# Optimization experiments

Measured on AMD Instinct MI355X. Metric: run time of the kernel, lower is better.

## Reference

```python
import jax, jax.numpy as jnp
import numpy as np

B, T, D = 2, 2048, 2048
H, KV = 16, 4
HD = D // H            # 128
N_REP = H // KV        # 4
KV_DIM = D * KV // H   # 512
ALIBI_W = 0.1


def _rotate_half(x):
    x1, x2 = jnp.split(x, 2, axis=-1)
    return jnp.concatenate([-x2, x1], axis=-1)


def _apply_rope(xq, xk, freqs_cis):
    # xq: [B,H,T,hd], xk: [B,KV,T,hd]; freqs_cis: [T, hd] (cos half | sin half)
    seq_len, head_dim = xq.shape[2], xq.shape[3]
    freqs = freqs_cis[:seq_len, :]
    half = head_dim // 2
    cos = jnp.repeat(freqs[:, :half], 2, axis=-1)[None, None]  # [1,1,T,hd]
    sin = jnp.repeat(freqs[:, half:], 2, axis=-1)[None, None]
    xq_out = xq * cos + _rotate_half(xq) * sin
    xk_out = xk * cos + _rotate_half(xk) * sin
    return xq_out, xk_out


def setup_inputs() -> dict:
    key = jax.random.key(0)
    ks = jax.random.split(key, 8)
    x = jax.random.normal(ks[0], (B, T, D), jnp.float32)
    # additive causal mask (0 on/below diag, -1e9 above)
    causal = jnp.tril(jnp.ones((T, T), jnp.bool_))
    mask = jnp.where(causal, 0.0, -1e9).astype(jnp.float32)[None, None]
    # RoPE table: first half cos, second half sin of t*theta
    inv_freq = 1.0 / (10000.0 ** (np.arange(0, HD, 2, dtype=np.float32) / HD))  # [hd/2]
    angles = jnp.arange(T, dtype=jnp.float32)[:, None] * jnp.asarray(inv_freq)[None, :]
    freqs_cis = jnp.concatenate([jnp.cos(angles), jnp.sin(angles)], axis=-1)  # [T, hd]
    # ALiBi bias: per-head slope * relative distance
    slopes = 2.0 ** (-8.0 * (jnp.arange(1, H + 1, dtype=jnp.float32) / H))  # [H]
    rel = (jnp.arange(T, dtype=jnp.float32)[None, :] - jnp.arange(T, dtype=jnp.float32)[:, None])
    alibi_bias = (-jnp.abs(rel)[None, None] * slopes[None, :, None, None]).astype(jnp.float32)
    std = 0.02
    Wq = std * jax.random.normal(ks[1], (D, D), jnp.float32)
    Wk = std * jax.random.normal(ks[2], (D, KV_DIM), jnp.float32)
    Wv = std * jax.random.normal(ks[3], (D, KV_DIM), jnp.float32)
    Wo = std * jax.random.normal(ks[4], (D, D), jnp.float32)
    return {"x": x, "mask": mask, "freqs_cis": freqs_cis, "alibi_bias": alibi_bias,
            "Wq": Wq, "Wk": Wk, "Wv": Wv, "Wo": Wo}


def reference(x, mask, freqs_cis, alibi_bias, Wq, Wk, Wv, Wo):
    b, t, d = x.shape
    q = (x @ Wq).reshape(b, t, H, HD).transpose(0, 2, 1, 3)      # [B,H,T,hd]
    k = (x @ Wk).reshape(b, t, KV, HD).transpose(0, 2, 1, 3)     # [B,KV,T,hd]
    v = (x @ Wv).reshape(b, t, KV, HD).transpose(0, 2, 1, 3)     # [B,KV,T,hd]
    q, k = _apply_rope(q, k, freqs_cis)
    # grouped-query scores: group query heads by kv head, avoid repeating K/V
    qg = q.reshape(b, KV, N_REP, t, HD)
    scores = jnp.einsum('bgrtd,bgsd->bgrts', qg, k) / jnp.sqrt(jnp.float32(HD))
    alibi = alibi_bias[:, :, :t, :t].reshape(1, KV, N_REP, t, t)
    scores = scores * (1.0 - ALIBI_W) + alibi * ALIBI_W
    scores = scores + mask[:, :, None, :t, :t]                   # broadcast [1,1,1,T,T]
    attn = jax.nn.softmax(scores.astype(jnp.float32), axis=-1).astype(x.dtype)
    out = jnp.einsum('bgrts,bgsd->bgrtd', attn, v)               # [B,KV,n_rep,T,hd]
    out = out.reshape(b, H, t, HD).transpose(0, 2, 1, 3).reshape(b, t, d)
    return out @ Wo
```

## Files before the change

### kernel.cpp

```cpp
#include <hip/hip_runtime.h>

#define T_SEQ 2048
#define D_MODEL 2048
#define NH 16
#define NKV 4
#define HEAD_DIM 128

typedef unsigned short u16;
typedef __attribute__((ext_vector_type(8))) short bf16x8;
typedef __attribute__((ext_vector_type(4))) float f32x4;

__device__ __forceinline__ float bf2f(u16 u) { return __uint_as_float(((unsigned)u) << 16); }
__device__ __forceinline__ u16 f2bf(float f) {
  unsigned x = __float_as_uint(f);
  return (u16)((x + 0x7FFFu + ((x >> 16) & 1u)) >> 16);
}
__device__ __forceinline__ float fexp2(float x) { return __builtin_amdgcn_exp2f(x); }

#define ASYNC_COPY16(g, l)                                                        \
  __builtin_amdgcn_global_load_lds((const __attribute__((address_space(1))) unsigned int*)(g), \
                                   (__attribute__((address_space(3))) unsigned int*)(l), 16, 0, 0)

#define BARRIER() do { asm volatile("" ::: "memory"); __builtin_amdgcn_s_barrier(); asm volatile("" ::: "memory"); } while (0)

__global__ void cast_kernel(const float* __restrict__ x, u16* __restrict__ y, int n4) {
  int i = blockIdx.x * 256 + threadIdx.x;
  if (i >= n4) return;
  const float4 v = reinterpret_cast<const float4*>(x)[i];
  unsigned p0 = (unsigned)f2bf(v.x) | ((unsigned)f2bf(v.y) << 16);
  unsigned p1 = (unsigned)f2bf(v.z) | ((unsigned)f2bf(v.w) << 16);
  reinterpret_cast<uint2*>(y)[i] = make_uint2(p0, p1);
}

__global__ void transpose_kernel(const float* __restrict__ W, u16* __restrict__ WT, int K, int N) {
  __shared__ float t[32][33];
  int n0 = blockIdx.x * 32, k0 = blockIdx.y * 32;
  int tx = threadIdx.x, ty = threadIdx.y;
#pragma unroll
  for (int i = 0; i < 32; i += 8)
    t[ty + i][tx] = W[(size_t)(k0 + ty + i) * N + n0 + tx];
  __syncthreads();
#pragma unroll
  for (int i = 0; i < 32; i += 8)
    WT[(size_t)(n0 + ty + i) * K + k0 + tx] = f2bf(t[tx][ty + i]);
}

__global__ void vt_kernel(const u16* __restrict__ vb, u16* __restrict__ vt, int vstride) {
  __shared__ u16 t[32][33];
  const int bg = blockIdx.z;
  const int b = bg >> 2, g = bg & 3;
  const int t0 = blockIdx.x * 32, n0 = blockIdx.y * 32;
  const int tx = threadIdx.x, ty = threadIdx.y;
#pragma unroll
  for (int i = 0; i < 32; i += 8)
    t[ty + i][tx] = vb[((size_t)(b * T_SEQ + t0 + ty + i)) * vstride + g * HEAD_DIM + n0 + tx];
  __syncthreads();
#pragma unroll
  for (int i = 0; i < 32; i += 8)
    vt[((size_t)(bg * HEAD_DIM + n0 + ty + i)) * T_SEQ + t0 + tx] = t[tx][ty + i];
}

template<int OUT_BF16>
__global__ __launch_bounds__(512, 1) void gemm256(const u16* __restrict__ A, const u16* __restrict__ BT,
                                                  void* __restrict__ Cv, int M, int N, int K) {
  __shared__ u16 S[4][256 * 64];
  const int tid = threadIdx.x;
  const int wave = tid >> 6, lane = tid & 63;
  const int lr = lane & 15, lg = lane >> 4;
  const int wm = wave >> 2, wn = wave & 3;
  const size_t arow0 = (size_t)blockIdx.y * 256;
  const size_t brow0 = (size_t)blockIdx.x * 256;
  const int NT = K >> 6;

  const int srow_in_w = lane >> 3;
  const int scol = ((lane & 7) ^ srow_in_w) << 3;

  f32x4 acc[8][4] = {};
  bf16x8 af[4][2], bf0[2][2], bf1[2][2];

  auto stage = [&](int mat, int half, int ktile, int buf) {
    if (ktile >= NT) return;
    const u16* gb = mat ? (BT + brow0 * K) : (A + arow0 * K);
    const int kcol = ktile << 6;
#pragma unroll
    for (int i = 0; i < 2; ++i) {
      const int row = half * 128 + i * 64 + wave * 8 + srow_in_w;
      const u16* src = gb + (size_t)row * K + kcol + scol;
      u16* dst = &S[buf * 2 + mat][(half * 128 + i * 64 + wave * 8) * 64];
      ASYNC_COPY16(src, dst);
    }
  };
  auto ldA = [&](int c, int mh) {
#pragma unroll
    for (int m4 = 0; m4 < 4; ++m4)
#pragma unroll
      for (int ks = 0; ks < 2; ++ks)
        af[m4][ks] = *reinterpret_cast<const bf16x8*>(
            &S[c * 2][(wm * 128 + (mh * 4 + m4) * 16 + lr) * 64 + ((((ks << 2) | lg) ^ (lane & 7)) << 3)]);
  };
  auto ldB = [&](int c, int nh, bf16x8 (*bfr)[2]) {
#pragma unroll
    for (int n2 = 0; n2 < 2; ++n2)
#pragma unroll
      for (int ks = 0; ks < 2; ++ks)
        bfr[n2][ks] = *reinterpret_cast<const bf16x8*>(
            &S[c * 2 + 1][(wn * 64 + (nh * 2 + n2) * 16 + lr) * 64 + ((((ks << 2) | lg) ^ (lane & 7)) << 3)]);
  };
  auto mfmaQ = [&](int mh, int nh, bf16x8 (*bfr)[2]) {
    __builtin_amdgcn_s_setprio(1);
#pragma unroll
    for (int m4 = 0; m4 < 4; ++m4)
#pragma unroll
      for (int n2 = 0; n2 < 2; ++n2)
#pragma unroll
        for (int ks = 0; ks < 2; ++ks)
          acc[mh * 4 + m4][nh * 2 + n2] = __builtin_amdgcn_mfma_f32_16x16x32_bf16(
              af[m4][ks], bfr[n2][ks], acc[mh * 4 + m4][nh * 2 + n2], 0, 0, 0);
    __builtin_amdgcn_s_setprio(0);
  };

  stage(0, 0, 0, 0); stage(0, 1, 0, 0); stage(1, 0, 0, 0); stage(1, 1, 0, 0);
  stage(1, 0, 1, 1); stage(0, 0, 1, 1);
  asm volatile("s_waitcnt vmcnt(4)" ::: "memory");
  BARRIER();

  for (int kt = 0; kt < NT; ++kt) {
    const int c = kt & 1;
    ldA(c, 0); ldB(c, 0, bf0);
    stage(0, 1, kt + 1, c ^ 1);
    BARRIER();
    mfmaQ(0, 0, bf0);
    BARRIER();
    ldB(c, 1, bf1);
    stage(1, 1, kt + 1, c ^ 1);
    BARRIER();
    mfmaQ(0, 1, bf1);
    BARRIER();
    ldA(c, 1);
    stage(1, 0, kt + 2, c);
    BARRIER();
    mfmaQ(1, 1, bf1);
    BARRIER();
    stage(0, 0, kt + 2, c);
    BARRIER();
    mfmaQ(1, 0, bf0);
    if (kt + 2 < NT) { asm volatile("s_waitcnt vmcnt(4)" ::: "memory"); }
    else             { asm volatile("s_waitcnt vmcnt(0)" ::: "memory"); }
    BARRIER();
  }

#pragma unroll
  for (int mf = 0; mf < 8; ++mf)
#pragma unroll
    for (int nf = 0; nf < 4; ++nf)
#pragma unroll
      for (int r = 0; r < 4; ++r) {
        size_t row = arow0 + wm * 128 + mf * 16 + lg * 4 + r;
        size_t col = brow0 + wn * 64 + nf * 16 + lr;
        if (OUT_BF16) ((u16*)Cv)[row * N + col] = f2bf(acc[mf][nf][r]);
        else          ((float*)Cv)[row * N + col] = acc[mf][nf][r];
      }
}

__global__ void rope_kernel(u16* __restrict__ q, const float* __restrict__ freqs, int log2nh,
                            int stride, int total) {
  int idx = blockIdx.x * 256 + threadIdx.x;
  if (idx >= total) return;
  int d = idx & 63;
  int h = (idx >> 6) & ((1 << log2nh) - 1);
  int row = idx >> (6 + log2nh);
  int t = row & (T_SEQ - 1);
  size_t base = (size_t)row * stride + (size_t)h * 128;
  float x1 = bf2f(q[base + d]);
  float x2 = bf2f(q[base + 64 + d]);
  const float* fr = freqs + (size_t)t * 128;
  int dh = d >> 1;
  float c1 = fr[dh],      s1 = fr[64 + dh];
  float c2 = fr[32 + dh], s2 = fr[96 + dh];
  q[base + d]      = f2bf(x1 * c1 - x2 * s1);
  q[base + 64 + d] = f2bf(x2 * c2 + x1 * s2);
}

__global__ __launch_bounds__(512) void attn_kernel(const u16* __restrict__ q, const u16* __restrict__ k,
                                                   const u16* __restrict__ vt, u16* __restrict__ o,
                                                   int qstride, int kstride) {
  __shared__ u16 Kl[2][64][136];
  __shared__ u16 Vl[2][128][72];
  __shared__ u16 Pl[8][16][72];
  const int b = blockIdx.z, h = blockIdx.y, pairIdx = blockIdx.x;
  const int g = h >> 2;
  const int tid = threadIdx.x, wave = tid >> 6, lane = tid & 63;
  const int lr = lane & 15, lg = lane >> 4;

  const float LOG2E = 1.44269504089f;
  const float qk_scale = 0.9f / sqrtf(128.f) * LOG2E;
  const float slope2   = 0.1f * fexp2(-0.5f * (h + 1)) * LOG2E;
  const float THR = 16.0f;

  const int krow = tid >> 3, kc0 = (tid & 7) * 16;
  const int vrow = tid >> 2, vc0 = (tid & 3) * 16;
  const u16* kbp = k + ((size_t)(b * T_SEQ + krow)) * kstride + g * HEAD_DIM + kc0;
  const u16* vbp = vt + ((size_t)((b * NKV + g) * HEAD_DIM + vrow)) * T_SEQ + vc0;

  float cb[4];
#pragma unroll
  for (int nt = 0; nt < 4; ++nt) cb[nt] = slope2 * (float)(nt * 16 + lr);

  for (int half = 0; half < 2; ++half) {
    const int qt = half ? (15 - pairIdx) : pairIdx;
    const int qbase = qt * 128;

    const u16* qp = q + ((size_t)(b * T_SEQ + qbase + wave * 16 + lr)) * qstride + h * HEAD_DIM;
    bf16x8 qf[4];
#pragma unroll
    for (int ks = 0; ks < 4; ++ks) qf[ks] = *reinterpret_cast<const bf16x8*>(qp + ks * 32 + lg * 8);

    f32x4 oa[8] = {};
    float m_r[4], l_r[4];
#pragma unroll
    for (int r = 0; r < 4; ++r) { m_r[r] = -1e30f; l_r[r] = 0.f; }

    const int ktmax = 2 * qt + 1;
    const int irow_min_w = qbase + wave * 16;
    const int irow_max_w = irow_min_w + 15;
    int cur = 0;

    __syncthreads();
    {
      bf16x8 k0a = *reinterpret_cast<const bf16x8*>(kbp);
      bf16x8 k0b = *reinterpret_cast<const bf16x8*>(kbp + 8);
      bf16x8 v0a = *reinterpret_cast<const bf16x8*>(vbp);
      bf16x8 v0b = *reinterpret_cast<const bf16x8*>(vbp + 8);
      *reinterpret_cast<bf16x8*>(&Kl[0][krow][kc0]) = k0a;
      *reinterpret_cast<bf16x8*>(&Kl[0][krow][kc0 + 8]) = k0b;
      *reinterpret_cast<bf16x8*>(&Vl[0][vrow][vc0]) = v0a;
      *reinterpret_cast<bf16x8*>(&Vl[0][vrow][vc0 + 8]) = v0b;
    }

    for (int kt = 0; kt <= ktmax; ++kt) {
      const int kbase = kt * 64;
      __syncthreads();

      const bool pf = (kt < ktmax);
      bf16x8 pk0, pk1, pv0, pv1;
      if (pf) {
        const u16* ks2p = kbp + (size_t)(kbase + 64) * kstride;
        pk0 = *reinterpret_cast<const bf16x8*>(ks2p);
        pk1 = *reinterpret_cast<const bf16x8*>(ks2p + 8);
        const u16* vs2p = vbp + kbase + 64;
        pv0 = *reinterpret_cast<const bf16x8*>(vs2p);
        pv1 = *reinterpret_cast<const bf16x8*>(vs2p + 8);
      }

      const bool compute = (kbase <= irow_max_w);
      if (compute) {
        f32x4 sa[4] = {};
#pragma unroll
        for (int nt = 0; nt < 4; ++nt)
#pragma unroll
          for (int ks = 0; ks < 4; ++ks)
            sa[nt] = __builtin_amdgcn_mfma_f32_16x16x32_bf16(
                qf[ks], *reinterpret_cast<const bf16x8*>(&Kl[cur][nt * 16 + lr][ks * 32 + lg * 8]), sa[nt], 0, 0, 0);

        const int i_row0 = irow_min_w + lg * 4;
        const float tb = slope2 * (float)kbase;
        float sv[4][4];
        float pmx[4] = {-1e30f, -1e30f, -1e30f, -1e30f};
        if (kbase + 63 <= irow_min_w) {
#pragma unroll
          for (int nt = 0; nt < 4; ++nt) {
            const float bias = cb[nt] + tb;
#pragma unroll
            for (int r = 0; r < 4; ++r) {
              float xv = fmaf(sa[nt][r], qk_scale, bias);
              sv[nt][r] = xv;
              pmx[r] = fmaxf(pmx[r], xv);
            }
          }
        } else {
#pragma unroll
          for (int nt = 0; nt < 4; ++nt) {
            const int jcol = kbase + nt * 16 + lr;
            const float bias = cb[nt] + tb;
#pragma unroll
            for (int r = 0; r < 4; ++r) {
              float xv = (jcol <= i_row0 + r) ? fmaf(sa[nt][r], qk_scale, bias) : -1e30f;
              sv[nt][r] = xv;
              pmx[r] = fmaxf(pmx[r], xv);
            }
          }
        }

        bool okl = true;
#pragma unroll
        for (int r = 0; r < 4; ++r) okl = okl && (pmx[r] <= m_r[r] + THR);
        if (__all(okl)) {
          float rs[4] = {0.f, 0.f, 0.f, 0.f};
#pragma unroll
          for (int nt = 0; nt < 4; ++nt)
#pragma unroll
            for (int r = 0; r < 4; ++r) {
              float p = fexp2(sv[nt][r] - m_r[r]);
              sv[nt][r] = p;
              rs[r] += p;
            }
#pragma unroll
          for (int r = 0; r < 4; ++r) l_r[r] += rs[r];
        } else {
#pragma unroll
          for (int mm = 1; mm < 16; mm <<= 1)
#pragma unroll
            for (int r = 0; r < 4; ++r) pmx[r] = fmaxf(pmx[r], __shfl_xor(pmx[r], mm, 64));
          float corr[4], rs[4];
#pragma unroll
          for (int r = 0; r < 4; ++r) {
            float mn = fmaxf(m_r[r], pmx[r]);
            corr[r] = fexp2(m_r[r] - mn);
            m_r[r] = mn;
            rs[r] = 0.f;
          }
#pragma unroll
          for (int nt = 0; nt < 4; ++nt)
#pragma unroll
            for (int r = 0; r < 4; ++r) {
              float p = fexp2(sv[nt][r] - m_r[r]);
              sv[nt][r] = p;
              rs[r] += p;
            }
#pragma unroll
          for (int r = 0; r < 4; ++r) l_r[r] = l_r[r] * corr[r] + rs[r];
#pragma unroll
          for (int t8 = 0; t8 < 8; ++t8)
#pragma unroll
            for (int r = 0; r < 4; ++r) oa[t8][r] *= corr[r];
        }

#pragma unroll
        for (int nt = 0; nt < 4; ++nt)
#pragma unroll
          for (int r = 0; r < 4; ++r)
            Pl[wave][lg * 4 + r][nt * 16 + lr] = f2bf(sv[nt][r]);
      }

      if (pf) {
        *reinterpret_cast<bf16x8*>(&Kl[cur ^ 1][krow][kc0]) = pk0;
        *reinterpret_cast<bf16x8*>(&Kl[cur ^ 1][krow][kc0 + 8]) = pk1;
        *reinterpret_cast<bf16x8*>(&Vl[cur ^ 1][vrow][vc0]) = pv0;
        *reinterpret_cast<bf16x8*>(&Vl[cur ^ 1][vrow][vc0 + 8]) = pv1;
      }

      if (compute) {
#pragma unroll
        for (int ht = 0; ht < 8; ++ht)
#pragma unroll
          for (int ks2 = 0; ks2 < 2; ++ks2) {
            bf16x8 pa = *reinterpret_cast<const bf16x8*>(&Pl[wave][lr][ks2 * 32 + lg * 8]);
            bf16x8 vb8 = *reinterpret_cast<const bf16x8*>(&Vl[cur][ht * 16 + lr][ks2 * 32 + lg * 8]);
            oa[ht] = __builtin_amdgcn_mfma_f32_16x16x32_bf16(pa, vb8, oa[ht], 0, 0, 0);
          }
      }
      cur ^= 1;
    }

#pragma unroll
    for (int mm = 1; mm < 16; mm <<= 1)
#pragma unroll
      for (int r = 0; r < 4; ++r) l_r[r] += __shfl_xor(l_r[r], mm, 64);

    u16* op = o + ((size_t)(b * T_SEQ + qbase + wave * 16)) * D_MODEL + h * HEAD_DIM;
#pragma unroll
    for (int r = 0; r < 4; ++r) {
      float inv = 1.0f / l_r[r];
#pragma unroll
      for (int ht = 0; ht < 8; ++ht)
        op[(size_t)(lg * 4 + r) * D_MODEL + ht * 16 + lr] = f2bf(oa[ht][r] * inv);
    }
  }
}

extern "C" void kernel_launch(void* const* d_in, const int* in_sizes, int n_in,
                              void* d_out, int out_size, void* d_ws, size_t ws_size,
                              hipStream_t stream) {
  (void)in_sizes; (void)n_in; (void)out_size; (void)ws_size;
  const float* x     = (const float*)d_in[0];
  const float* freqs = (const float*)d_in[2];
  const float* Wq    = (const float*)d_in[4];
  const float* Wk    = (const float*)d_in[5];
  const float* Wv    = (const float*)d_in[6];
  const float* Wo    = (const float*)d_in[7];
  float* out = (float*)d_out;
  char* ws = (char*)d_ws;
  const size_t MB = 1024 * 1024;
  u16* xb   = (u16*)(ws);
  u16* qkvT = (u16*)(ws + 16 * MB);
  u16* WoT  = (u16*)(ws + 28 * MB);
  u16* qkv  = (u16*)(ws + 36 * MB);
  u16* vtb  = (u16*)(ws + 16 * MB);
  const int M = 2 * T_SEQ;
  const int NQKV = 3072;

  cast_kernel<<<(M * D_MODEL / 4 + 255) / 256, 256, 0, stream>>>(x, xb, M * D_MODEL / 4);
  dim3 tb(32, 8);
  transpose_kernel<<<dim3(2048 / 32, 2048 / 32), tb, 0, stream>>>(Wq, qkvT, 2048, 2048);
  transpose_kernel<<<dim3(512 / 32, 2048 / 32), tb, 0, stream>>>(Wk, qkvT + (size_t)2048 * 2048, 2048, 512);
  transpose_kernel<<<dim3(512 / 32, 2048 / 32), tb, 0, stream>>>(Wv, qkvT + (size_t)2560 * 2048, 2048, 512);
  transpose_kernel<<<dim3(2048 / 32, 2048 / 32), tb, 0, stream>>>(Wo, WoT, 2048, 2048);

  gemm256<1><<<dim3(NQKV / 256, M / 256), 512, 0, stream>>>(xb, qkvT, qkv, M, NQKV, 2048);

  rope_kernel<<<(M * NH * 64) / 256, 256, 0, stream>>>(qkv, freqs, 4, NQKV, M * NH * 64);
  rope_kernel<<<(M * NKV * 64) / 256, 256, 0, stream>>>(qkv + 2048, freqs, 2, NQKV, M * NKV * 64);

  vt_kernel<<<dim3(T_SEQ / 32, HEAD_DIM / 32, 2 * NKV), tb, 0, stream>>>(qkv + 2560, vtb, NQKV);

  attn_kernel<<<dim3(8, NH, 2), 512, 0, stream>>>(qkv, qkv + 2048, vtb, xb, NQKV, NQKV);

  gemm256<0><<<dim3(2048 / 256, M / 256), 512, 0, stream>>>(xb, WoT, out, M, 2048, 2048);
}
```

Measured before the change: 237.3 us.

## Retile GEMMs to fill 256 CUs with swizzled 1D grid, merge small launches

Generalizes the GEMM kernel over tile shape and picks 256x192 tiles for the QKV projection and 128x256 tiles for the output projection, so each GEMM launches exactly 256 workgroups with an XCD-aware block swizzle instead of 192 or 128 blocks. It also fuses the four weight transposes into one launch and the two RoPE launches into one to cut launch overhead. Smaller or non-square tiles lower per-block reuse and change the prefetch depth, which may lengthen each block's main loop.

```diff
diff --git a/kernel.cpp b/kernel.cpp
--- a/kernel.cpp
+++ b/kernel.cpp
@@ -22,6 +22,13 @@
                                    (__attribute__((address_space(3))) unsigned int*)(l), 16, 0, 0)
 
 #define BARRIER() do { asm volatile("" ::: "memory"); __builtin_amdgcn_s_barrier(); asm volatile("" ::: "memory"); } while (0)
+
+template<int N> __device__ __forceinline__ void vmwait() {
+  if constexpr (N == 0) asm volatile("s_waitcnt vmcnt(0)" ::: "memory");
+  else if constexpr (N == 3) asm volatile("s_waitcnt vmcnt(3)" ::: "memory");
+  else if constexpr (N == 4) asm volatile("s_waitcnt vmcnt(4)" ::: "memory");
+  else if constexpr (N == 5) asm volatile("s_waitcnt vmcnt(5)" ::: "memory");
+}
 
 __global__ void cast_kernel(const float* __restrict__ x, u16* __restrict__ y, int n4) {
   int i = blockIdx.x * 256 + threadIdx.x;
@@ -32,17 +39,26 @@
   reinterpret_cast<uint2*>(y)[i] = make_uint2(p0, p1);
 }
 
-__global__ void transpose_kernel(const float* __restrict__ W, u16* __restrict__ WT, int K, int N) {
+__global__ void transpose4_kernel(const float* __restrict__ Wq, const float* __restrict__ Wk,
+                                  const float* __restrict__ Wv, const float* __restrict__ Wo,
+                                  u16* __restrict__ qkvT, u16* __restrict__ WoT) {
   __shared__ float t[32][33];
-  int n0 = blockIdx.x * 32, k0 = blockIdx.y * 32;
-  int tx = threadIdx.x, ty = threadIdx.y;
+  const int m = blockIdx.z;
+  const float* W; u16* WT; int N;
+  if (m == 0)      { W = Wq; WT = qkvT;                         N = 2048; }
+  else if (m == 1) { W = Wk; WT = qkvT + (size_t)2048 * 2048;   N = 512;  }
+  else if (m == 2) { W = Wv; WT = qkvT + (size_t)2560 * 2048;   N = 512;  }
+  else             { W = Wo; WT = WoT;                          N = 2048; }
+  const int n0 = blockIdx.x * 32, k0 = blockIdx.y * 32;
+  if (n0 >= N) return;
+  const int tx = threadIdx.x, ty = threadIdx.y;
 #pragma unroll
   for (int i = 0; i < 32; i += 8)
     t[ty + i][tx] = W[(size_t)(k0 + ty + i) * N + n0 + tx];
   __syncthreads();
 #pragma unroll
   for (int i = 0; i < 32; i += 8)
-    WT[(size_t)(n0 + ty + i) * K + k0 + tx] = f2bf(t[tx][ty + i]);
+    WT[(size_t)(n0 + ty + i) * 2048 + k0 + tx] = f2bf(t[tx][ty + i]);
 }
 
 __global__ void vt_kernel(const u16* __restrict__ vb, u16* __restrict__ vt, int vstride) {
@@ -60,125 +76,150 @@
     vt[((size_t)(bg * HEAD_DIM + n0 + ty + i)) * T_SEQ + t0 + tx] = t[tx][ty + i];
 }
 
-template<int OUT_BF16>
-__global__ __launch_bounds__(512, 1) void gemm256(const u16* __restrict__ A, const u16* __restrict__ BT,
-                                                  void* __restrict__ Cv, int M, int N, int K) {
-  __shared__ u16 S[4][256 * 64];
+template<int BM, int BN, int WM, int WN, int EA, int EB, int OUT_BF16>
+__global__ __launch_bounds__(512, 1) void gemm_dp(const u16* __restrict__ A, const u16* __restrict__ BT,
+                                                  void* __restrict__ Cv, int M, int N, int K, int nbx) {
+  constexpr int PA = BM / 64, PB = BN / 64;
+  constexpr int E = EA + EB;
+  constexpr int FM = BM / WM / 16, FN = BN / WN / 16;
+  static_assert(FM % 2 == 0 && FN % 2 == 0, "quadrant split");
+  __shared__ u16 SA[2][BM * 64];
+  __shared__ u16 SB[2][BN * 64];
   const int tid = threadIdx.x;
   const int wave = tid >> 6, lane = tid & 63;
   const int lr = lane & 15, lg = lane >> 4;
-  const int wm = wave >> 2, wn = wave & 3;
-  const size_t arow0 = (size_t)blockIdx.y * 256;
-  const size_t brow0 = (size_t)blockIdx.x * 256;
+  const int wm = wave / WN, wn = wave % WN;
+  const int nwg = gridDim.x;
+  const int bid = blockIdx.x;
+  const int swz = (bid & 7) * (nwg >> 3) + (bid >> 3);
+  const int bx = swz % nbx, by = swz / nbx;
+  const size_t arow0 = (size_t)by * BM;
+  const size_t brow0 = (size_t)bx * BN;
   const int NT = K >> 6;
 
-  const int srow_in_w = lane >> 3;
-  const int scol = ((lane & 7) ^ srow_in_w) << 3;
-
-  f32x4 acc[8][4] = {};
-  bf16x8 af[4][2], bf0[2][2], bf1[2][2];
-
-  auto stage = [&](int mat, int half, int ktile, int buf) {
+  const int srow = tid >> 3;
+  const int scol = ((tid & 7) ^ (srow & 7)) << 3;
+
+  f32x4 acc[FM][FN] = {};
+  bf16x8 af[FM / 2][2], bf0[FN / 2][2], bf1[FN / 2][2];
+
+  const u16* Abase = A + arow0 * K;
+  const u16* Bbase = BT + brow0 * K;
+
+  auto stageA = [&](int p, int ktile, int buf) {
     if (ktile >= NT) return;
-    const u16* gb = mat ? (BT + brow0 * K) : (A + arow0 * K);
-    const int kcol = ktile << 6;
-#pragma unroll
-    for (int i = 0; i < 2; ++i) {
-      const int row = half * 128 + i * 64 + wave * 8 + srow_in_w;
-      const u16* src = gb + (size_t)row * K + kcol + scol;
-      u16* dst = &S[buf * 2 + mat][(half * 128 + i * 64 + wave * 8) * 64];
-      ASYNC_COPY16(src, dst);
-    }
+    const u16* src = Abase + (size_t)(p * 64 + srow) * K + (ktile << 6) + scol;
+    ASYNC_COPY16(src, &SA[buf][(p * 64 + wave * 8) * 64]);
+  };
+  auto stageB = [&](int p, int ktile, int buf) {
+    if (ktile >= NT) return;
+    const u16* src = Bbase + (size_t)(p * 64 + srow) * K + (ktile << 6) + scol;
+    ASYNC_COPY16(src, &SB[buf][(p * 64 + wave * 8) * 64]);
   };
   auto ldA = [&](int c, int mh) {
 #pragma unroll
-    for (int m4 = 0; m4 < 4; ++m4)
-#pragma unroll
-      for (int ks = 0; ks < 2; ++ks)
-        af[m4][ks] = *reinterpret_cast<const bf16x8*>(
-            &S[c * 2][(wm * 128 + (mh * 4 + m4) * 16 + lr) * 64 + ((((ks << 2) | lg) ^ (lane & 7)) << 3)]);
+    for (int mf = 0; mf < FM / 2; ++mf)
+#pragma unroll
+      for (int ks = 0; ks < 2; ++ks) {
+        const int row = wm * (BM / WM) + (mh * (FM / 2) + mf) * 16 + lr;
+        const int slot = ((ks << 2) | lg) ^ (lr & 7);
+        af[mf][ks] = *reinterpret_cast<const bf16x8*>(&SA[c][row * 64 + (slot << 3)]);
+      }
   };
   auto ldB = [&](int c, int nh, bf16x8 (*bfr)[2]) {
 #pragma unroll
-    for (int n2 = 0; n2 < 2; ++n2)
-#pragma unroll
-      for (int ks = 0; ks < 2; ++ks)
-        bfr[n2][ks] = *reinterpret_cast<const bf16x8*>(
-            &S[c * 2 + 1][(wn * 64 + (nh * 2 + n2) * 16 + lr) * 64 + ((((ks << 2) | lg) ^ (lane & 7)) << 3)]);
+    for (int nf = 0; nf < FN / 2; ++nf)
+#pragma unroll
+      for (int ks = 0; ks < 2; ++ks) {
+        const int row = wn * (BN / WN) + (nh * (FN / 2) + nf) * 16 + lr;
+        const int slot = ((ks << 2) | lg) ^ (lr & 7);
+        bfr[nf][ks] = *reinterpret_cast<const bf16x8*>(&SB[c][row * 64 + (slot << 3)]);
+      }
   };
-  auto mfmaQ = [&](int mh, int nh, bf16x8 (*bfr)[2]) {
+  auto mq = [&](int mh, int nh, bf16x8 (*bfr)[2]) {
     __builtin_amdgcn_s_setprio(1);
 #pragma unroll
-    for (int m4 = 0; m4 < 4; ++m4)
-#pragma unroll
-      for (int n2 = 0; n2 < 2; ++n2)
+    for (int mf = 0; mf < FM / 2; ++mf)
+#pragma unroll
+      for (int nf = 0; nf < FN / 2; ++nf)
 #pragma unroll
         for (int ks = 0; ks < 2; ++ks)
-          acc[mh * 4 + m4][nh * 2 + n2] = __builtin_amdgcn_mfma_f32_16x16x32_bf16(
-              af[m4][ks], bfr[n2][ks], acc[mh * 4 + m4][nh * 2 + n2], 0, 0, 0);
+          acc[mh * (FM / 2) + mf][nh * (FN / 2) + nf] = __builtin_amdgcn_mfma_f32_16x16x32_bf16(
+              af[mf][ks], bfr[nf][ks], acc[mh * (FM / 2) + mf][nh * (FN / 2) + nf], 0, 0, 0);
     __builtin_amdgcn_s_setprio(0);
   };
 
-  stage(0, 0, 0, 0); stage(0, 1, 0, 0); stage(1, 0, 0, 0); stage(1, 1, 0, 0);
-  stage(1, 0, 1, 1); stage(0, 0, 1, 1);
-  asm volatile("s_waitcnt vmcnt(4)" ::: "memory");
+#pragma unroll
+  for (int p = 0; p < PA; ++p) stageA(p, 0, 0);
+#pragma unroll
+  for (int p = 0; p < PB; ++p) stageB(p, 0, 0);
+#pragma unroll
+  for (int p = 0; p < EB; ++p) stageB(p, 1, 1);
+#pragma unroll
+  for (int p = 0; p < EA; ++p) stageA(p, 1, 1);
+  vmwait<E>();
   BARRIER();
 
   for (int kt = 0; kt < NT; ++kt) {
     const int c = kt & 1;
     ldA(c, 0); ldB(c, 0, bf0);
-    stage(0, 1, kt + 1, c ^ 1);
-    BARRIER();
-    mfmaQ(0, 0, bf0);
+#pragma unroll
+    for (int p = EB; p < PB; ++p) stageB(p, kt + 1, c ^ 1);
+    BARRIER();
+    mq(0, 0, bf0);
     BARRIER();
     ldB(c, 1, bf1);
-    stage(1, 1, kt + 1, c ^ 1);
-    BARRIER();
-    mfmaQ(0, 1, bf1);
+#pragma unroll
+    for (int p = EA; p < PA; ++p) stageA(p, kt + 1, c ^ 1);
+    BARRIER();
+    mq(0, 1, bf1);
     BARRIER();
     ldA(c, 1);
-    stage(1, 0, kt + 2, c);
-    BARRIER();
-    mfmaQ(1, 1, bf1);
-    BARRIER();
-    stage(0, 0, kt + 2, c);
-    BARRIER();
-    mfmaQ(1, 0, bf0);
-    if (kt + 2 < NT) { asm volatile("s_waitcnt vmcnt(4)" ::: "memory"); }
-    else             { asm volatile("s_waitcnt vmcnt(0)" ::: "memory"); }
+#pragma unroll
+    for (int p = 0; p < EB; ++p) stageB(p, kt + 2, c);
+    BARRIER();
+    mq(1, 1, bf1);
+    BARRIER();
+#pragma unroll
+    for (int p = 0; p < EA; ++p) stageA(p, kt + 2, c);
+    BARRIER();
+    mq(1, 0, bf0);
+    if (kt + 2 < NT) vmwait<E>(); else vmwait<0>();
     BARRIER();
   }
 
 #pragma unroll
-  for (int mf = 0; mf < 8; ++mf)
-#pragma unroll
-    for (int nf = 0; nf < 4; ++nf)
+  for (int mf = 0; mf < FM; ++mf)
+#pragma unroll
+    for (int nf = 0; nf < FN; ++nf)
 #pragma unroll
       for (int r = 0; r < 4; ++r) {
-        size_t row = arow0 + wm * 128 + mf * 16 + lg * 4 + r;
-        size_t col = brow0 + wn * 64 + nf * 16 + lr;
+        size_t row = arow0 + wm * (BM / WM) + mf * 16 + lg * 4 + r;
+        size_t col = brow0 + wn * (BN / WN) + nf * 16 + lr;
         if (OUT_BF16) ((u16*)Cv)[row * N + col] = f2bf(acc[mf][nf][r]);
         else          ((float*)Cv)[row * N + col] = acc[mf][nf][r];
       }
 }
 
-__global__ void rope_kernel(u16* __restrict__ q, const float* __restrict__ freqs, int log2nh,
-                            int stride, int total) {
+__global__ void rope2_kernel(u16* __restrict__ qkv, const float* __restrict__ freqs) {
+  const int QT = 4096 * NH * 64;
   int idx = blockIdx.x * 256 + threadIdx.x;
-  if (idx >= total) return;
+  u16* p; int log2nh;
+  if (idx < QT) { p = qkv; log2nh = 4; }
+  else          { p = qkv + 2048; log2nh = 2; idx -= QT; }
   int d = idx & 63;
   int h = (idx >> 6) & ((1 << log2nh) - 1);
   int row = idx >> (6 + log2nh);
   int t = row & (T_SEQ - 1);
-  size_t base = (size_t)row * stride + (size_t)h * 128;
-  float x1 = bf2f(q[base + d]);
-  float x2 = bf2f(q[base + 64 + d]);
+  size_t base = (size_t)row * 3072 + (size_t)h * 128;
+  float x1 = bf2f(p[base + d]);
+  float x2 = bf2f(p[base + 64 + d]);
   const float* fr = freqs + (size_t)t * 128;
   int dh = d >> 1;
   float c1 = fr[dh],      s1 = fr[64 + dh];
   float c2 = fr[32 + dh], s2 = fr[96 + dh];
-  q[base + d]      = f2bf(x1 * c1 - x2 * s1);
-  q[base + 64 + d] = f2bf(x2 * c2 + x1 * s2);
+  p[base + d]      = f2bf(x1 * c1 - x2 * s1);
+  p[base + 64 + d] = f2bf(x2 * c2 + x1 * s2);
 }
 
 __global__ __launch_bounds__(512) void attn_kernel(const u16* __restrict__ q, const u16* __restrict__ k,
@@ -401,19 +442,15 @@
 
   cast_kernel<<<(M * D_MODEL / 4 + 255) / 256, 256, 0, stream>>>(x, xb, M * D_MODEL / 4);
   dim3 tb(32, 8);
-  transpose_kernel<<<dim3(2048 / 32, 2048 / 32), tb, 0, stream>>>(Wq, qkvT, 2048, 2048);
-  transpose_kernel<<<dim3(512 / 32, 2048 / 32), tb, 0, stream>>>(Wk, qkvT + (size_t)2048 * 2048, 2048, 512);
-  transpose_kernel<<<dim3(512 / 32, 2048 / 32), tb, 0, stream>>>(Wv, qkvT + (size_t)2560 * 2048, 2048, 512);
-  transpose_kernel<<<dim3(2048 / 32, 2048 / 32), tb, 0, stream>>>(Wo, WoT, 2048, 2048);
-
-  gemm256<1><<<dim3(NQKV / 256, M / 256), 512, 0, stream>>>(xb, qkvT, qkv, M, NQKV, 2048);
-
-  rope_kernel<<<(M * NH * 64) / 256, 256, 0, stream>>>(qkv, freqs, 4, NQKV, M * NH * 64);
-  rope_kernel<<<(M * NKV * 64) / 256, 256, 0, stream>>>(qkv + 2048, freqs, 2, NQKV, M * NKV * 64);
+  transpose4_kernel<<<dim3(64, 64, 4), tb, 0, stream>>>(Wq, Wk, Wv, Wo, qkvT, WoT);
+
+  gemm_dp<256, 192, 4, 2, 2, 2, 1><<<256, 512, 0, stream>>>(xb, qkvT, qkv, M, NQKV, 2048, NQKV / 192);
+
+  rope2_kernel<<<(M * NH * 64 + M * NKV * 64) / 256, 256, 0, stream>>>(qkv, freqs);
 
   vt_kernel<<<dim3(T_SEQ / 32, HEAD_DIM / 32, 2 * NKV), tb, 0, stream>>>(qkv + 2560, vtb, NQKV);
 
   attn_kernel<<<dim3(8, NH, 2), 512, 0, stream>>>(qkv, qkv + 2048, vtb, xb, NQKV, NQKV);
 
-  gemm256<0><<<dim3(2048 / 256, M / 256), 512, 0, stream>>>(xb, WoT, out, M, 2048, 2048);
-}
+  gemm_dp<128, 256, 2, 4, 1, 2, 0><<<256, 512, 0, stream>>>(xb, WoT, out, M, 2048, 2048, 2048 / 256);
+}
```

Result: faster. 212.0 us, median of 2 (-10.6%).
